# Kernel optimization log

Hardware: AMD Instinct MI355X
Metric: run time of the kernel (lower is better)

## Reference

```python
import jax, jax.numpy as jnp
import numpy as np

B, CIN, H, W = 2, 32, 64, 64
COUT, K, PAD = 32, 3, 1
KK = K * K
PRED_W = COUT * CIN * KK  # 9216 dynamic-weight channels
PRED_OUT = PRED_W + COUT  # + per-pixel bias
EPS = 1e-12


def setup_inputs() -> dict:
    key = jax.random.key(0)
    k1, k2 = jax.random.split(key)
    x = jax.random.normal(k1, (B, CIN, H, W), dtype=jnp.float32)
    # 1x1-conv predictor weights (Conv2d(in_ch, pred_out, 1)), fan-in scaled
    Wp = jax.random.normal(k2, (PRED_OUT, CIN), dtype=jnp.float32) / np.sqrt(CIN).astype(np.float32)
    bp = jnp.zeros((PRED_OUT,), dtype=jnp.float32)
    return {"x": x, "Wp": Wp, "bp": bp}


def _unfold3x3(x):
    # F.unfold with k=3, pad=1, stride=1, dilation=1 -> (B, Cin, 9, L), c slowest then (kh, kw)
    xp = jnp.pad(x, ((0, 0), (0, 0), (PAD, PAD), (PAD, PAD)))
    patches = jnp.stack(
        [xp[:, :, i:i + H, j:j + W] for i in range(K) for j in range(K)], axis=2
    )  # (B, Cin, 9, H, W)
    return patches.reshape(B, CIN, KK, H * W)


def _l2norm(v, axis):
    n = jnp.sqrt(jnp.sum(v * v, axis=axis, keepdims=True))
    return v / jnp.maximum(n, EPS)


def reference(x, Wp, bp):
    L = H * W
    patches = _unfold3x3(x)  # (B, Cin, 9, L)
    # 1x1 conv predictor (stride=1 path -> operates on x directly)
    pred = jnp.einsum('oc,bchw->bohw', Wp, x) + bp[None, :, None, None]  # (B, PRED_OUT, H, W)
    dyn_w = pred[:, :PRED_W].reshape(B, COUT, CIN, KK, L)
    dyn_b = pred[:, PRED_W:].reshape(B, COUT, L)
    # norm_pred: L2-normalize over Cin axis, then over k*k axis
    dyn_w = _l2norm(dyn_w, axis=2)
    dyn_w = _l2norm(dyn_w, axis=3)
    out = jnp.einsum('bockl,bckl->bol', dyn_w, patches) + dyn_b  # (B, Cout, L)
    return out.reshape(B, COUT, H, W)
```

## Files before the change

kernel.cpp:

```cpp
#include <hip/hip_runtime.h>

#define TPB 256

typedef __attribute__((ext_vector_type(8))) short short8;
typedef __attribute__((ext_vector_type(4))) float f32x4;

__device__ __forceinline__ unsigned f2bf_pk(float a, float b) {
  return ((__float_as_uint(a) + 0x8000u) >> 16) | ((__float_as_uint(b) + 0x8000u) & 0xffff0000u);
}
__device__ __forceinline__ float bflo(unsigned v) { return __uint_as_float(v << 16); }
__device__ __forceinline__ float bfhi(unsigned v) { return __uint_as_float(v & 0xffff0000u); }

__global__ void prep_kernel(const float* __restrict__ Wp, unsigned* __restrict__ Wq) {
  int idx = blockIdx.x * blockDim.x + threadIdx.x;
  if (idx >= 32 * 18 * 64 * 4) return;
  int j2   = idx & 3;
  int lane = (idx >> 2) & 63;
  int rt   = (idx >> 8) % 18;
  int o    = (idx >> 8) / 18;
  int m16 = lane & 15, kq = lane >> 4;
  int row = o * 288 + (m16 >> 2) * 72 + rt * 4 + (m16 & 3);
  const float* src = Wp + row * 32 + kq * 8 + j2 * 2;
  Wq[idx] = f2bf_pk(src[0], src[1]);
}

template <bool USE_WQ>
__global__ __launch_bounds__(TPB, 3) void dppc5_kernel(
    const float* __restrict__ x, const float* __restrict__ Wp,
    const float* __restrict__ bp, const unsigned* __restrict__ Wq,
    float* __restrict__ out) {
  __shared__ __align__(16) unsigned short xrow[3 * 32 * 68];
  __shared__ __align__(16) float bp_s[4 * 288];
  __shared__ __align__(16) float Wb_s[4 * 32];
  __shared__ float bias4[4];

  const int tid = threadIdx.x;
  const int bid = blockIdx.x;
  const int og  = bid & 7;
  const int t   = bid >> 3;
  const int b   = t >> 6;
  const int h   = t & 63;

  for (int i = tid; i < 96; i += TPB) {
    unsigned* row = (unsigned*)&xrow[i * 68];
    row[0] = 0;
    row[33] = 0;
  }
  for (int i = tid; i < 1536; i += TPB) {
    int r = i >> 9, c = (i >> 4) & 31, w4 = i & 15;
    int hh = h - 1 + r;
    unsigned* dst = (unsigned*)&xrow[(r * 32 + c) * 68 + 2 + w4 * 4];
    if ((unsigned)hh < 64u) {
      const float4 v = *(const float4*)(x + (((b * 32 + c) * 64 + hh) * 64 + w4 * 4));
      dst[0] = f2bf_pk(v.x, v.y);
      dst[1] = f2bf_pk(v.z, v.w);
    } else {
      dst[0] = 0u;
      dst[1] = 0u;
    }
  }
  for (int i = tid; i < 1152; i += TPB) bp_s[i] = bp[og * 1152 + i];
  if (tid < 128) Wb_s[tid] = Wp[(9216 + og * 4 + (tid >> 5)) * 32 + (tid & 31)];
  if (tid < 4) bias4[tid] = bp[9216 + og * 4 + tid];
  __syncthreads();

  const int lane = tid & 63;
  const int wv   = tid >> 6;
  const int m16  = lane & 15, kq = lane >> 4;
  const int px   = wv * 16 + m16;

  union { short8 v; unsigned short s[8]; } bf_;
#pragma unroll
  for (int j = 0; j < 8; ++j)
    bf_.s[j] = xrow[(32 + kq * 8 + j) * 68 + 2 + px];
  const short8 bfrag = bf_.v;

  unsigned patchp[36];
#pragma unroll
  for (int i = 0; i < 36; ++i) patchp[i] = 0;
#pragma unroll
  for (int c8 = 0; c8 < 8; ++c8)
#pragma unroll
    for (int kk = 0; kk < 9; ++kk) {
      const int kh = kk / 3, kw = kk - kh * 3;
      unsigned v = (unsigned)xrow[(kh * 32 + kq * 8 + c8) * 68 + 1 + kw + px];
      const int idx = c8 * 9 + kk;
      patchp[idx >> 1] |= (idx & 1) ? (v << 16) : v;
    }

#pragma unroll 1
  for (int oo = 0; oo < 4; ++oo) {
    const int o = og * 4 + oo;

    f32x4 acc[18];
    if (USE_WQ) {
      const short8* wq = (const short8*)Wq + (o * 18) * 64 + lane;
#pragma unroll
      for (int rt = 0; rt < 18; ++rt) {
        const f32x4 bb = *(const f32x4*)&bp_s[oo * 288 + kq * 72 + rt * 4];
        acc[rt] = __builtin_amdgcn_mfma_f32_16x16x32_bf16(wq[rt * 64], bfrag, bb, 0, 0, 0);
      }
    } else {
      const float* ab = Wp + (o * 288 + (m16 >> 2) * 72 + (m16 & 3)) * 32 + kq * 8;
#pragma unroll
      for (int rt = 0; rt < 18; ++rt) {
        const float* ap = ab + rt * 4 * 32;
        float4 a0 = *(const float4*)ap;
        float4 a1 = *(const float4*)(ap + 4);
        union { short8 v; unsigned u[4]; } af;
        af.u[0] = f2bf_pk(a0.x, a0.y);
        af.u[1] = f2bf_pk(a0.z, a0.w);
        af.u[2] = f2bf_pk(a1.x, a1.y);
        af.u[3] = f2bf_pk(a1.z, a1.w);
        const f32x4 bb = *(const f32x4*)&bp_s[oo * 288 + kq * 72 + rt * 4];
        acc[rt] = __builtin_amdgcn_mfma_f32_16x16x32_bf16(af.v, bfrag, bb, 0, 0, 0);
      }
    }

    float rinv[9];
#pragma unroll
    for (int kk = 0; kk < 9; ++kk) rinv[kk] = 0.f;
#pragma unroll
    for (int c8 = 0; c8 < 8; ++c8)
#pragma unroll
      for (int kk = 0; kk < 9; ++kk) {
        const int idx = c8 * 9 + kk;
        const float v = acc[idx >> 2][idx & 3];
        rinv[kk] += v * v;
      }
#pragma unroll
    for (int kk = 0; kk < 9; ++kk) {
      float s = rinv[kk];
      s += __shfl_xor(s, 16);
      s += __shfl_xor(s, 32);
      rinv[kk] = rsqrtf(fmaxf(s, 1e-24f));
    }

    const f32x4 wb0 = *(const f32x4*)&Wb_s[oo * 32 + kq * 8];
    const f32x4 wb1 = *(const f32x4*)&Wb_s[oo * 32 + kq * 8 + 4];
    float oacc = 0.f;
#pragma unroll
    for (int c8 = 0; c8 < 8; ++c8) {
      float s2 = 0.f, dot = 0.f;
#pragma unroll
      for (int kk = 0; kk < 9; ++kk) {
        const int idx = c8 * 9 + kk;
        const float tv = acc[idx >> 2][idx & 3] * rinv[kk];
        s2 += tv * tv;
        const float pv = (idx & 1) ? bfhi(patchp[idx >> 1]) : bflo(patchp[idx >> 1]);
        dot += tv * pv;
      }
      oacc += rsqrtf(fmaxf(s2, 1e-24f)) * dot;
      const int idc = c8 * 9 + 4;
      const float xc = (idc & 1) ? bfhi(patchp[idc >> 1]) : bflo(patchp[idc >> 1]);
      const float wbv = (c8 < 4) ? ((const float*)&wb0)[c8] : ((const float*)&wb1)[c8 - 4];
      oacc += wbv * xc;
    }
    oacc += __shfl_xor(oacc, 16);
    oacc += __shfl_xor(oacc, 32);
    if (kq == 0)
      out[((b * 32 + o) * 64 + h) * 64 + px] = oacc + bias4[oo];
  }
}

extern "C" void kernel_launch(void* const* d_in, const int* in_sizes, int n_in,
                              void* d_out, int out_size, void* d_ws, size_t ws_size,
                              hipStream_t stream) {
  const float* x  = (const float*)d_in[0];
  const float* Wp = (const float*)d_in[1];
  const float* bp = (const float*)d_in[2];
  float* out = (float*)d_out;
  const size_t wq_bytes = (size_t)32 * 18 * 64 * 8 * 2;
  if (ws_size >= wq_bytes) {
    prep_kernel<<<576, 256, 0, stream>>>(Wp, (unsigned*)d_ws);
    dppc5_kernel<true><<<1024, TPB, 0, stream>>>(x, Wp, bp, (const unsigned*)d_ws, out);
  } else {
    dppc5_kernel<false><<<1024, TPB, 0, stream>>>(x, Wp, bp, nullptr, out);
  }
}
```

Before: 88.75 us.

## Double-buffer per-output weights via async global-to-LDS DMA and transpose x tile layout

Per-output bf16 weight fragments are now staged into a double-buffered LDS region with global_load_lds, and the next output's weights are prefetched while the current one computes. The loop gets a barrier per iteration. The x row tile changes to a pixel-major, channel-inner layout so the B fragment and the 3x3 patch values load as 16-byte vector reads instead of scalar gathers. The kernel also drops from 3 to 2 waves-per-EU launch bounds to fit the extra ~36KB of LDS, which reduces occupancy and adds synchronization.

```diff
diff --git a/kernel.cpp b/kernel.cpp
--- a/kernel.cpp
+++ b/kernel.cpp
@@ -10,6 +10,12 @@
 }
 __device__ __forceinline__ float bflo(unsigned v) { return __uint_as_float(v << 16); }
 __device__ __forceinline__ float bfhi(unsigned v) { return __uint_as_float(v & 0xffff0000u); }
+
+__device__ __forceinline__ void dma16(const void* g, void* l) {
+  __builtin_amdgcn_global_load_lds(
+      (const __attribute__((address_space(1))) unsigned*)g,
+      (__attribute__((address_space(3))) unsigned*)l, 16, 0, 0);
+}
 
 __global__ void prep_kernel(const float* __restrict__ Wp, unsigned* __restrict__ Wq) {
   int idx = blockIdx.x * blockDim.x + threadIdx.x;
@@ -25,11 +31,12 @@
 }
 
 template <bool USE_WQ>
-__global__ __launch_bounds__(TPB, 3) void dppc5_kernel(
+__global__ __launch_bounds__(TPB, 2) void dppc8_kernel(
     const float* __restrict__ x, const float* __restrict__ Wp,
     const float* __restrict__ bp, const unsigned* __restrict__ Wq,
     float* __restrict__ out) {
-  __shared__ __align__(16) unsigned short xrow[3 * 32 * 68];
+  __shared__ __align__(16) unsigned short xrow2[3 * 66 * 40];
+  __shared__ __align__(16) char wqbuf[2][18432];
   __shared__ __align__(16) float bp_s[4 * 288];
   __shared__ __align__(16) float Wb_s[4 * 32];
   __shared__ float bias4[4];
@@ -41,23 +48,29 @@
   const int b   = t >> 6;
   const int h   = t & 63;
 
-  for (int i = tid; i < 96; i += TPB) {
-    unsigned* row = (unsigned*)&xrow[i * 68];
-    row[0] = 0;
-    row[33] = 0;
+  const char* wq_g = (const char*)Wq + (size_t)(og * 4) * 18432;
+
+  if (USE_WQ) {
+    for (int c = tid; c < 1152; c += TPB)
+      dma16(wq_g + c * 16, wqbuf[0] + c * 16);
+  }
+
+  for (int i = tid; i < 120; i += TPB) {
+    int p = i / 20, w = i % 20;
+    ((unsigned*)xrow2)[(((p >> 1) * 66 + ((p & 1) ? 65 : 0)) * 20) + w] = 0;
   }
   for (int i = tid; i < 1536; i += TPB) {
-    int r = i >> 9, c = (i >> 4) & 31, w4 = i & 15;
+    int px_ = i & 63, c4 = (i >> 6) & 7, r = i >> 9;
     int hh = h - 1 + r;
-    unsigned* dst = (unsigned*)&xrow[(r * 32 + c) * 68 + 2 + w4 * 4];
+    unsigned w0 = 0, w1 = 0;
     if ((unsigned)hh < 64u) {
-      const float4 v = *(const float4*)(x + (((b * 32 + c) * 64 + hh) * 64 + w4 * 4));
-      dst[0] = f2bf_pk(v.x, v.y);
-      dst[1] = f2bf_pk(v.z, v.w);
-    } else {
-      dst[0] = 0u;
-      dst[1] = 0u;
+      const float* xp = x + ((b * 32 + c4 * 4) * 64 + hh) * 64 + px_;
+      float f0 = xp[0], f1 = xp[4096], f2 = xp[8192], f3 = xp[12288];
+      w0 = f2bf_pk(f0, f1);
+      w1 = f2bf_pk(f2, f3);
     }
+    uint2* dst = (uint2*)&xrow2[(r * 66 + 1 + px_) * 40 + c4 * 4];
+    *dst = make_uint2(w0, w1);
   }
   for (int i = tid; i < 1152; i += TPB) bp_s[i] = bp[og * 1152 + i];
   if (tid < 128) Wb_s[tid] = Wp[(9216 + og * 4 + (tid >> 5)) * 32 + (tid & 31)];
@@ -69,36 +82,37 @@
   const int m16  = lane & 15, kq = lane >> 4;
   const int px   = wv * 16 + m16;
 
-  union { short8 v; unsigned short s[8]; } bf_;
+  const short8 bfrag = *(const short8*)&xrow2[(66 + 1 + px) * 40 + kq * 8];
+
+  unsigned patch2[36];
 #pragma unroll
-  for (int j = 0; j < 8; ++j)
-    bf_.s[j] = xrow[(32 + kq * 8 + j) * 68 + 2 + px];
-  const short8 bfrag = bf_.v;
-
-  unsigned patchp[36];
-#pragma unroll
-  for (int i = 0; i < 36; ++i) patchp[i] = 0;
-#pragma unroll
-  for (int c8 = 0; c8 < 8; ++c8)
-#pragma unroll
-    for (int kk = 0; kk < 9; ++kk) {
-      const int kh = kk / 3, kw = kk - kh * 3;
-      unsigned v = (unsigned)xrow[(kh * 32 + kq * 8 + c8) * 68 + 1 + kw + px];
-      const int idx = c8 * 9 + kk;
-      patchp[idx >> 1] |= (idx & 1) ? (v << 16) : v;
-    }
+  for (int kk = 0; kk < 9; ++kk) {
+    const int kh = kk / 3, kw = kk - kh * 3;
+    const uint4 tp = *(const uint4*)&xrow2[(kh * 66 + kw + px) * 40 + kq * 8];
+    patch2[kk * 4 + 0] = tp.x;
+    patch2[kk * 4 + 1] = tp.y;
+    patch2[kk * 4 + 2] = tp.z;
+    patch2[kk * 4 + 3] = tp.w;
+  }
 
 #pragma unroll 1
   for (int oo = 0; oo < 4; ++oo) {
     const int o = og * 4 + oo;
+    const int buf = oo & 1;
+
+    if (USE_WQ && oo < 3) {
+      const char* g = wq_g + (size_t)(oo + 1) * 18432;
+      for (int c = tid; c < 1152; c += TPB)
+        dma16(g + c * 16, wqbuf[buf ^ 1] + c * 16);
+    }
 
     f32x4 acc[18];
     if (USE_WQ) {
-      const short8* wq = (const short8*)Wq + (o * 18) * 64 + lane;
 #pragma unroll
       for (int rt = 0; rt < 18; ++rt) {
+        const short8 a = *(const short8*)(wqbuf[buf] + (rt * 64 + lane) * 16);
         const f32x4 bb = *(const f32x4*)&bp_s[oo * 288 + kq * 72 + rt * 4];
-        acc[rt] = __builtin_amdgcn_mfma_f32_16x16x32_bf16(wq[rt * 64], bfrag, bb, 0, 0, 0);
+        acc[rt] = __builtin_amdgcn_mfma_f32_16x16x32_bf16(a, bfrag, bb, 0, 0, 0);
       }
     } else {
       const float* ab = Wp + (o * 288 + (m16 >> 2) * 72 + (m16 & 3)) * 32 + kq * 8;
@@ -136,8 +150,6 @@
       rinv[kk] = rsqrtf(fmaxf(s, 1e-24f));
     }
 
-    const f32x4 wb0 = *(const f32x4*)&Wb_s[oo * 32 + kq * 8];
-    const f32x4 wb1 = *(const f32x4*)&Wb_s[oo * 32 + kq * 8 + 4];
     float oacc = 0.f;
 #pragma unroll
     for (int c8 = 0; c8 < 8; ++c8) {
@@ -147,19 +159,21 @@
         const int idx = c8 * 9 + kk;
         const float tv = acc[idx >> 2][idx & 3] * rinv[kk];
         s2 += tv * tv;
-        const float pv = (idx & 1) ? bfhi(patchp[idx >> 1]) : bflo(patchp[idx >> 1]);
+        const unsigned wd = patch2[kk * 4 + (c8 >> 1)];
+        const float pv = (c8 & 1) ? bfhi(wd) : bflo(wd);
         dot += tv * pv;
       }
       oacc += rsqrtf(fmaxf(s2, 1e-24f)) * dot;
-      const int idc = c8 * 9 + 4;
-      const float xc = (idc & 1) ? bfhi(patchp[idc >> 1]) : bflo(patchp[idc >> 1]);
-      const float wbv = (c8 < 4) ? ((const float*)&wb0)[c8] : ((const float*)&wb1)[c8 - 4];
-      oacc += wbv * xc;
+      const unsigned wc = patch2[16 + (c8 >> 1)];
+      const float xc = (c8 & 1) ? bfhi(wc) : bflo(wc);
+      oacc += Wb_s[oo * 32 + kq * 8 + c8] * xc;
     }
     oacc += __shfl_xor(oacc, 16);
     oacc += __shfl_xor(oacc, 32);
     if (kq == 0)
       out[((b * 32 + o) * 64 + h) * 64 + px] = oacc + bias4[oo];
+
+    if (oo < 3) __syncthreads();
   }
 }
 
@@ -173,8 +187,8 @@
   const size_t wq_bytes = (size_t)32 * 18 * 64 * 8 * 2;
   if (ws_size >= wq_bytes) {
     prep_kernel<<<576, 256, 0, stream>>>(Wp, (unsigned*)d_ws);
-    dppc5_kernel<true><<<1024, TPB, 0, stream>>>(x, Wp, bp, (const unsigned*)d_ws, out);
+    dppc8_kernel<true><<<1024, TPB, 0, stream>>>(x, Wp, bp, (const unsigned*)d_ws, out);
   } else {
-    dppc5_kernel<false><<<1024, TPB, 0, stream>>>(x, Wp, bp, nullptr, out);
+    dppc8_kernel<false><<<1024, TPB, 0, stream>>>(x, Wp, bp, nullptr, out);
   }
 }
```

Measured after the change: 82.76 us. 6.8% less time.
